# Optimization experiments

Hardware: AMD Instinct MI355X
Metric: run time of the kernel (lower is better)

Reference implementation:

```python
import jax, jax.numpy as jnp
import numpy as np

D_MODEL = 1024
NUM_HEADS = 16
HEAD_DIM = D_MODEL // NUM_HEADS  # 64
# NOTE: the original module passes scale=attention_head_size, so scores are
# MULTIPLIED by head_dim (64), not divided by sqrt(head_dim). Faithful quirk.
SCALE = float(HEAD_DIM)


def setup_inputs() -> dict:
    key = jax.random.key(0)
    ks = jax.random.split(key, 6)
    bs, s, d = 2, 2048, D_MODEL
    q = jax.random.normal(ks[0], (bs, s, d), dtype=jnp.float32)
    k = jax.random.normal(ks[1], (bs, s, d), dtype=jnp.float32)
    v = jax.random.normal(ks[2], (bs, s, d), dtype=jnp.float32)
    # nn.Linear weights, shape (out, in); no bias (qkv_bias=False)
    init = 1.0 / np.sqrt(d)
    Wq = jax.random.uniform(ks[3], (d, d), jnp.float32, -init, init)
    Wk = jax.random.uniform(ks[4], (d, d), jnp.float32, -init, init)
    Wv = jax.random.uniform(ks[5], (d, d), jnp.float32, -init, init)
    return {"q": q, "k": k, "v": v, "Wq": Wq, "Wk": Wk, "Wv": Wv}


def _split_heads(x):
    bs, s, _ = x.shape
    return x.reshape(bs, s, NUM_HEADS, HEAD_DIM).transpose(0, 2, 1, 3)  # bhsd


def reference(q, k, v, Wq, Wk, Wv):
    bs, s, d = q.shape
    qh = _split_heads(q @ Wq.T)  # [b,h,s,hd]
    kh = _split_heads(k @ Wk.T)
    vh = _split_heads(v @ Wv.T)
    sims = jnp.einsum('bhqd,bhkd->bhqk', qh, kh) * SCALE
    attn = jax.nn.softmax(sims, axis=-1)
    out = jnp.einsum('bhqk,bhkd->bhqd', attn, vh)  # [b,h,s,hd]
    out = out.transpose(0, 2, 1, 3).reshape(bs, s, d)
    return out
```

## Files before the change

kernel.cpp:

```cpp
#include <hip/hip_runtime.h>


typedef _Float16 half4 __attribute__((ext_vector_type(4)));
typedef _Float16 half8 __attribute__((ext_vector_type(8)));
typedef float floatx4 __attribute__((ext_vector_type(4)));

#define MFMA_F16(a, b, c) __builtin_amdgcn_mfma_f32_16x16x32_f16((a), (b), (c), 0, 0, 0)

constexpr int SEQ = 2048;
constexpr int DM = 1024;
constexpr int NH = 16;
constexpr int HD = 64;
constexpr float QSCALE = 92.33248261689366f;

__device__ __forceinline__ void gl2lds16(const _Float16* g, _Float16* l) {
  __builtin_amdgcn_global_load_lds(
      (const __attribute__((address_space(1))) void*)g,
      (__attribute__((address_space(3))) void*)l, 16, 0, 0);
}

__device__ inline void split4(const float4 f, half4& h, half4& l) {
  h[0] = (_Float16)f.x; l[0] = (_Float16)(f.x - (float)h[0]);
  h[1] = (_Float16)f.y; l[1] = (_Float16)(f.y - (float)h[1]);
  h[2] = (_Float16)f.z; l[2] = (_Float16)(f.z - (float)h[2]);
  h[3] = (_Float16)f.w; l[3] = (_Float16)(f.w - (float)h[3]);
}

__global__ __launch_bounds__(256) void convert_all(
    const float* __restrict__ q, const float* __restrict__ k,
    const float* __restrict__ v, const float* __restrict__ Wq,
    const float* __restrict__ Wk, const float* __restrict__ Wv,
    _Float16* __restrict__ xq_h, _Float16* __restrict__ xq_l,
    _Float16* __restrict__ xk_h, _Float16* __restrict__ xk_l,
    _Float16* __restrict__ xv_h,
    _Float16* __restrict__ Wqh, _Float16* __restrict__ Wql,
    _Float16* __restrict__ Wkh, _Float16* __restrict__ Wkl,
    _Float16* __restrict__ Wvh)
{
  const int bid = blockIdx.x;
  const float* src; _Float16* dh; _Float16* dl; int do_lo, i0;
  if (bid < 4096)       { src = q;  dh = xq_h; dl = xq_l; do_lo = 1; i0 = bid; }
  else if (bid < 8192)  { src = k;  dh = xk_h; dl = xk_l; do_lo = 1; i0 = bid - 4096; }
  else if (bid < 12288) { src = v;  dh = xv_h; dl = xv_h; do_lo = 0; i0 = bid - 8192; }
  else if (bid < 13312) { src = Wq; dh = Wqh;  dl = Wql;  do_lo = 1; i0 = bid - 12288; }
  else if (bid < 14336) { src = Wk; dh = Wkh;  dl = Wkl;  do_lo = 1; i0 = bid - 13312; }
  else                  { src = Wv; dh = Wvh;  dl = Wvh;  do_lo = 0; i0 = bid - 14336; }
  const int idx = i0 * 256 + threadIdx.x;
  float4 f = ((const float4*)src)[idx];
  half4 h, l; split4(f, h, l);
  *(half4*)(dh + (size_t)idx * 4) = h;
  if (do_lo) *(half4*)(dl + (size_t)idx * 4) = l;
}

__global__ __launch_bounds__(256, 1) void proj3_kernel(
    const _Float16* __restrict__ xq_h, const _Float16* __restrict__ xq_l,
    const _Float16* __restrict__ xk_h, const _Float16* __restrict__ xk_l,
    const _Float16* __restrict__ xv_h,
    const _Float16* __restrict__ Wqh, const _Float16* __restrict__ Wql,
    const _Float16* __restrict__ Wkh, const _Float16* __restrict__ Wkl,
    const _Float16* __restrict__ Wvh,
    _Float16* __restrict__ qh_hi, _Float16* __restrict__ qh_lo,
    _Float16* __restrict__ kh_hi, _Float16* __restrict__ kh_lo,
    _Float16* __restrict__ vhT)
{
  __shared__ __align__(16) _Float16 Ahs[128][64];
  __shared__ __align__(16) _Float16 Als[128][64];
  __shared__ __align__(16) _Float16 Bhs[128][64];
  __shared__ __align__(16) _Float16 Bls[128][64];

  const int z = blockIdx.z;
  const _Float16 *Ahg, *Alg, *Bhg, *Blg;
  _Float16 *yh, *yl;
  float scale; int three;
  if (z == 0)      { Ahg = xq_h; Alg = xq_l; Bhg = Wqh; Blg = Wql;
                     yh = qh_hi; yl = qh_lo; scale = QSCALE; three = 1; }
  else if (z == 1) { Ahg = xk_h; Alg = xk_l; Bhg = Wkh; Blg = Wkl;
                     yh = kh_hi; yl = kh_lo; scale = 1.0f; three = 1; }
  else             { Ahg = xv_h; Alg = xv_h; Bhg = Wvh; Blg = Wvh;
                     yh = vhT;   yl = vhT;   scale = 1.0f; three = 0; }

  const int tid = threadIdx.x;
  const int bm = blockIdx.x;
  const int bn = blockIdx.y;
  const int lane = tid & 63, l15 = lane & 15, quad = lane >> 4;
  const int w = tid >> 6, wm = w >> 1, wn = w & 1;

  const int r8 = lane >> 3;
  const int cp8 = (((lane & 7) ^ r8)) * 8;
  int grow[4]; _Float16* la[4]; _Float16* lal[4]; _Float16* lb[4]; _Float16* lbl[4];
  #pragma unroll
  for (int i = 0; i < 4; i++) {
    const int g = w * 4 + i;
    grow[i] = g * 8 + r8;
    la[i]  = &Ahs[0][0] + g * 512;
    lal[i] = &Als[0][0] + g * 512;
    lb[i]  = &Bhs[0][0] + g * 512;
    lbl[i] = &Bls[0][0] + g * 512;
  }

  floatx4 acc[4][4];
  #pragma unroll
  for (int mt = 0; mt < 4; mt++)
    #pragma unroll
    for (int nt = 0; nt < 4; nt++)
      acc[mt][nt] = (floatx4){0.f, 0.f, 0.f, 0.f};

  for (int kk = 0; kk < DM; kk += 64) {
    __syncthreads();
    #pragma unroll
    for (int i = 0; i < 4; i++) {
      const size_t ga = (size_t)(bm * 128 + grow[i]) * DM + kk + cp8;
      const size_t gb = (size_t)(bn * 128 + grow[i]) * DM + kk + cp8;
      gl2lds16(Ahg + ga, la[i]);
      gl2lds16(Bhg + gb, lb[i]);
      if (three) {
        gl2lds16(Alg + ga, lal[i]);
        gl2lds16(Blg + gb, lbl[i]);
      }
    }
    __syncthreads();

    #pragma unroll
    for (int kc = 0; kc < 2; kc++) {
      const int swz = ((kc * 4 + quad) ^ (l15 & 7)) * 8;
      half8 ah[4], bh_[4], al[4], bl[4];
      #pragma unroll
      for (int t = 0; t < 4; t++) {
        ah[t]  = *(const half8*)&Ahs[wm * 64 + t * 16 + l15][swz];
        bh_[t] = *(const half8*)&Bhs[wn * 64 + t * 16 + l15][swz];
        if (three) {
          al[t] = *(const half8*)&Als[wm * 64 + t * 16 + l15][swz];
          bl[t] = *(const half8*)&Bls[wn * 64 + t * 16 + l15][swz];
        }
      }
      if (three) {
        #pragma unroll
        for (int mt = 0; mt < 4; mt++)
          #pragma unroll
          for (int nt = 0; nt < 4; nt++) {
            floatx4 t0 = MFMA_F16(ah[mt], bh_[nt], acc[mt][nt]);
            t0 = MFMA_F16(ah[mt], bl[nt], t0);
            acc[mt][nt] = MFMA_F16(al[mt], bh_[nt], t0);
          }
      } else {
        #pragma unroll
        for (int mt = 0; mt < 4; mt++)
          #pragma unroll
          for (int nt = 0; nt < 4; nt++)
            acc[mt][nt] = MFMA_F16(ah[mt], bh_[nt], acc[mt][nt]);
      }
    }
  }

  if (three) {
    #pragma unroll
    for (int mt = 0; mt < 4; mt++)
      #pragma unroll
      for (int nt = 0; nt < 4; nt++)
        #pragma unroll
        for (int r = 0; r < 4; r++) {
          int gm = bm * 128 + wm * 64 + mt * 16 + quad * 4 + r;
          int gn = bn * 128 + wn * 64 + nt * 16 + l15;
          int b = gm >> 11, s = gm & 2047;
          int h = gn >> 6, d = gn & 63;
          size_t idx = ((size_t)(b * NH + h) * SEQ + s) * HD + d;
          float val = acc[mt][nt][r] * scale;
          _Float16 hi = (_Float16)val;
          yh[idx] = hi;
          yl[idx] = (_Float16)(val - (float)hi);
        }
  } else {
    const int b = bm >> 4;
    const int h = bn * 2 + wn;
    const int bh = b * NH + h;
    const int sbase = (bm & 15) * 128 + wm * 64;
    _Float16* vt = vhT + (size_t)bh * HD * SEQ;
    #pragma unroll
    for (int mt = 0; mt < 4; mt++) {
      const int pos = sbase + (mt >> 1) * 32 + quad * 8 + (mt & 1) * 4;
      #pragma unroll
      for (int nt = 0; nt < 4; nt++) {
        const int d = nt * 16 + l15;
        half4 hv;
        hv[0] = (_Float16)acc[mt][nt][0];
        hv[1] = (_Float16)acc[mt][nt][1];
        hv[2] = (_Float16)acc[mt][nt][2];
        hv[3] = (_Float16)acc[mt][nt][3];
        *(half4*)(vt + (size_t)d * SEQ + pos) = hv;
      }
    }
  }
}

__global__ __launch_bounds__(256, 4) void flash_kernel(
    const _Float16* __restrict__ qh_hi, const _Float16* __restrict__ qh_lo,
    const _Float16* __restrict__ kh_hi, const _Float16* __restrict__ kh_lo,
    const _Float16* __restrict__ vhT, float* __restrict__ Op, float2* __restrict__ ml)
{
  __shared__ __align__(16) _Float16 Kh[2][64][64];
  __shared__ __align__(16) _Float16 Kl[2][64][64];
  __shared__ __align__(16) _Float16 Vt[64][64];

  const int id = blockIdx.x;
  const int seq_ = id >> 3;
  const int bh = (id & 7) + 8 * (seq_ & 3);
  const int rem = seq_ >> 2;
  const int qb = rem & 15;
  const int kh = rem >> 4;
  const int tid = threadIdx.x;
  const int wq = tid >> 6;
  const int lane = tid & 63, l15 = lane & 15, quad = lane >> 4;

  const size_t bh_off = (size_t)bh * SEQ * HD;
  const _Float16* __restrict__ kh_p = kh_hi + bh_off;
  const _Float16* __restrict__ kl_p = kh_lo + bh_off;
  const _Float16* __restrict__ vt_p = vhT + (size_t)bh * HD * SEQ;
  const int qrow0 = qb * 128 + wq * 32;

  half8 bqh[2][2], bql[2][2];
  #pragma unroll
  for (int g = 0; g < 2; g++) {
    const _Float16* qp_h = qh_hi + bh_off + (size_t)(qrow0 + g * 16 + l15) * HD;
    const _Float16* qp_l = qh_lo + bh_off + (size_t)(qrow0 + g * 16 + l15) * HD;
    #pragma unroll
    for (int kc = 0; kc < 2; kc++) {
      bqh[g][kc] = *(const half8*)(qp_h + kc * 32 + quad * 8);
      bql[g][kc] = *(const half8*)(qp_l + kc * 32 + quad * 8);
    }
  }

  const int r8 = lane >> 3;
  const int cp8 = ((lane & 7) ^ r8) * 8;

  float m_[2] = {-3.0e38f, -3.0e38f};
  float l_[2] = {0.f, 0.f};
  floatx4 Oacc[2][4];
  #pragma unroll
  for (int g = 0; g < 2; g++)
    #pragma unroll
    for (int nd = 0; nd < 4; nd++) Oacc[g][nd] = (floatx4){0.f, 0.f, 0.f, 0.f};

  const int kt0 = kh * 16;
  {
    const int kbase = kt0 * 64;
    #pragma unroll
    for (int i = 0; i < 2; i++) {
      const int g = wq * 2 + i;
      const int r = g * 8 + r8;
      gl2lds16(kh_p + (size_t)(kbase + r) * HD + cp8, &Kh[0][0][0] + g * 512);
      gl2lds16(kl_p + (size_t)(kbase + r) * HD + cp8, &Kl[0][0][0] + g * 512);
    }
  }

  for (int kt = kt0; kt < kt0 + 16; kt++) {
    const int cur = kt & 1;
    const int kbase = kt * 64;
    __syncthreads();

    #pragma unroll
    for (int i = 0; i < 2; i++) {
      const int g = wq * 2 + i;
      const int r = g * 8 + r8;
      gl2lds16(vt_p + (size_t)r * SEQ + kbase + cp8, &Vt[0][0] + g * 512);
    }
    if (kt + 1 < kt0 + 16) {
      const int kb2 = (kt + 1) * 64, nxt = cur ^ 1;
      #pragma unroll
      for (int i = 0; i < 2; i++) {
        const int g = wq * 2 + i;
        const int r = g * 8 + r8;
        gl2lds16(kh_p + (size_t)(kb2 + r) * HD + cp8, &Kh[nxt][0][0] + g * 512);
        gl2lds16(kl_p + (size_t)(kb2 + r) * HD + cp8, &Kl[nxt][0][0] + g * 512);
      }
    }

    floatx4 sacc[2][4];
    const int r7 = l15 & 7;
    #pragma unroll
    for (int nt = 0; nt < 4; nt++) {
      half8 akh0 = *(const half8*)&Kh[cur][nt * 16 + l15][((0 * 4 + quad) ^ r7) * 8];
      half8 akh1 = *(const half8*)&Kh[cur][nt * 16 + l15][((1 * 4 + quad) ^ r7) * 8];
      half8 akl0 = *(const half8*)&Kl[cur][nt * 16 + l15][((0 * 4 + quad) ^ r7) * 8];
      half8 akl1 = *(const half8*)&Kl[cur][nt * 16 + l15][((1 * 4 + quad) ^ r7) * 8];
      #pragma unroll
      for (int g = 0; g < 2; g++) {
        floatx4 s4 = (floatx4){0.f, 0.f, 0.f, 0.f};
        s4 = MFMA_F16(akh0, bqh[g][0], s4);
        s4 = MFMA_F16(akh1, bqh[g][1], s4);
        s4 = MFMA_F16(akh0, bql[g][0], s4);
        s4 = MFMA_F16(akh1, bql[g][1], s4);
        s4 = MFMA_F16(akl0, bqh[g][0], s4);
        s4 = MFMA_F16(akl1, bqh[g][1], s4);
        sacc[g][nt] = s4;
      }
    }

    float alpha2[2];
    half8 bp8g[2][2];
    #pragma unroll
    for (int g = 0; g < 2; g++) {
      float rmax = sacc[g][0][0];
      #pragma unroll
      for (int nt = 0; nt < 4; nt++)
        #pragma unroll
        for (int r = 0; r < 4; r++) rmax = fmaxf(rmax, sacc[g][nt][r]);
      rmax = fmaxf(rmax, __shfl_xor(rmax, 16, 64));
      rmax = fmaxf(rmax, __shfl_xor(rmax, 32, 64));
      const float mnew = fmaxf(m_[g], rmax);
      alpha2[g] = exp2f(m_[g] - mnew);
      m_[g] = mnew;

      float rsum = 0.f;
      #pragma unroll
      for (int nt = 0; nt < 4; nt++)
        #pragma unroll
        for (int r = 0; r < 4; r++) {
          float p = exp2f(sacc[g][nt][r] - mnew);
          sacc[g][nt][r] = p;
          rsum += p;
        }
      rsum += __shfl_xor(rsum, 16, 64);
      rsum += __shfl_xor(rsum, 32, 64);
      l_[g] = l_[g] * alpha2[g] + rsum;

      #pragma unroll
      for (int kc = 0; kc < 2; kc++)
        #pragma unroll
        for (int j = 0; j < 8; j++)
          bp8g[g][kc][j] = (_Float16)sacc[g][2 * kc + (j >> 2)][j & 3];
    }

    __syncthreads();

    half8 av[4][2];
    #pragma unroll
    for (int nd = 0; nd < 4; nd++) {
      av[nd][0] = *(const half8*)&Vt[nd * 16 + l15][((0 * 4 + quad) ^ r7) * 8];
      av[nd][1] = *(const half8*)&Vt[nd * 16 + l15][((1 * 4 + quad) ^ r7) * 8];
    }

    #pragma unroll
    for (int g = 0; g < 2; g++) {
      #pragma unroll
      for (int nd = 0; nd < 4; nd++) {
        Oacc[g][nd][0] *= alpha2[g]; Oacc[g][nd][1] *= alpha2[g];
        Oacc[g][nd][2] *= alpha2[g]; Oacc[g][nd][3] *= alpha2[g];
        Oacc[g][nd] = MFMA_F16(av[nd][0], bp8g[g][0], Oacc[g][nd]);
        Oacc[g][nd] = MFMA_F16(av[nd][1], bp8g[g][1], Oacc[g][nd]);
      }
    }
  }

  const size_t fqbase = (size_t)bh * SEQ + qrow0;
  #pragma unroll
  for (int g = 0; g < 2; g++) {
    const size_t fq = fqbase + g * 16 + l15;
    float* ob = Op + ((size_t)kh * 65536 + fq) * HD;
    #pragma unroll
    for (int nd = 0; nd < 4; nd++) {
      float4 vv;
      vv.x = Oacc[g][nd][0]; vv.y = Oacc[g][nd][1];
      vv.z = Oacc[g][nd][2]; vv.w = Oacc[g][nd][3];
      *(float4*)(ob + nd * 16 + quad * 4) = vv;
    }
    if (quad == 0) ml[kh * 65536 + fq] = make_float2(m_[g], l_[g]);
  }
}

__global__ __launch_bounds__(256) void merge_kernel(const float* __restrict__ Op,
                                                    const float2* __restrict__ ml,
                                                    float* __restrict__ out)
{
  const int tid = threadIdx.x;
  const int fq = blockIdx.x * 64 + (tid >> 2);
  const int dp = (tid & 3) * 16;
  float2 m0 = ml[fq], m1 = ml[65536 + fq];
  float M = fmaxf(m0.x, m1.x);
  float w0 = exp2f(m0.x - M), w1 = exp2f(m1.x - M);
  float rinv = 1.0f / (m0.y * w0 + m1.y * w1);
  int bh = fq >> 11, s = fq & 2047, b = bh >> 4, h = bh & 15;
  float* ob = out + ((size_t)(b * SEQ + s)) * DM + h * HD + dp;
  const float* p0 = Op + (size_t)fq * HD + dp;
  const float* p1 = p0 + (size_t)65536 * HD;
  #pragma unroll
  for (int j = 0; j < 4; j++) {
    float4 a = *(const float4*)(p0 + 4 * j);
    float4 c = *(const float4*)(p1 + 4 * j);
    float4 r;
    r.x = (a.x * w0 + c.x * w1) * rinv;
    r.y = (a.y * w0 + c.y * w1) * rinv;
    r.z = (a.z * w0 + c.z * w1) * rinv;
    r.w = (a.w * w0 + c.w * w1) * rinv;
    *(float4*)(ob + 4 * j) = r;
  }
}

extern "C" void kernel_launch(void* const* d_in, const int* in_sizes, int n_in,
                              void* d_out, int out_size, void* d_ws, size_t ws_size,
                              hipStream_t stream) {
  const float* q  = (const float*)d_in[0];
  const float* k  = (const float*)d_in[1];
  const float* v  = (const float*)d_in[2];
  const float* Wq = (const float*)d_in[3];
  const float* Wk = (const float*)d_in[4];
  const float* Wv = (const float*)d_in[5];
  float* out = (float*)d_out;

  char* W = (char*)d_ws;
  const size_t MiB = 1ull << 20;
  _Float16* qh_hi = (_Float16*)(W + 0 * MiB);
  _Float16* qh_lo = (_Float16*)(W + 8 * MiB);
  _Float16* kh_hi = (_Float16*)(W + 16 * MiB);
  _Float16* kh_lo = (_Float16*)(W + 24 * MiB);
  _Float16* vhT   = (_Float16*)(W + 32 * MiB);
  _Float16* xq_h  = (_Float16*)(W + 48 * MiB);
  _Float16* xq_l  = (_Float16*)(W + 56 * MiB);
  _Float16* xk_h  = (_Float16*)(W + 64 * MiB);
  _Float16* xk_l  = (_Float16*)(W + 72 * MiB);
  _Float16* xv_h  = (_Float16*)(W + 80 * MiB);
  _Float16* Wqh   = (_Float16*)(W + 88 * MiB);
  _Float16* Wql   = (_Float16*)(W + 90 * MiB);
  _Float16* Wkh   = (_Float16*)(W + 92 * MiB);
  _Float16* Wkl   = (_Float16*)(W + 94 * MiB);
  _Float16* Wvh   = (_Float16*)(W + 96 * MiB);
  float*    Op    = (float*)  (W + 40 * MiB);
  float2*   mlp   = (float2*) (W + 98 * MiB);

  convert_all<<<15360, 256, 0, stream>>>(q, k, v, Wq, Wk, Wv,
                                         xq_h, xq_l, xk_h, xk_l, xv_h,
                                         Wqh, Wql, Wkh, Wkl, Wvh);
  proj3_kernel<<<dim3(32, 8, 3), 256, 0, stream>>>(
      xq_h, xq_l, xk_h, xk_l, xv_h, Wqh, Wql, Wkh, Wkl, Wvh,
      qh_hi, qh_lo, kh_hi, kh_lo, vhT);
  flash_kernel<<<1024, 256, 0, stream>>>(qh_hi, qh_lo, kh_hi, kh_lo, vhT, Op, mlp);
  merge_kernel<<<1024, 256, 0, stream>>>(Op, mlp, out);
}
```

Baseline: 286.6 us.

## Stage projection epilogue through LDS, compute softmax row sums via MFMA

The Q/K projection epilogue now stages the hi/lo fp16 results in shared memory and writes them to global as coalesced 16-byte vectors instead of scattered 2-byte stores. In the attention kernel the row-sum reduction (VALU adds plus two shuffles) is replaced by an MFMA against a ones vector over the fp16 probabilities, which moves work to the matrix unit. The row max now uses a three-input max pattern. The risks are that the sum is taken over fp16-rounded probabilities, and that the epilogue adds several barriers.

```diff
diff --git a/kernel.cpp b/kernel.cpp
--- a/kernel.cpp
+++ b/kernel.cpp
@@ -12,6 +12,10 @@
 constexpr int NH = 16;
 constexpr int HD = 64;
 constexpr float QSCALE = 92.33248261689366f;
+
+__device__ __forceinline__ float fmax3(float a, float b, float c) {
+  return fmaxf(fmaxf(a, b), c);
+}
 
 __device__ __forceinline__ void gl2lds16(const _Float16* g, _Float16* l) {
   __builtin_amdgcn_global_load_lds(
@@ -63,10 +67,11 @@
     _Float16* __restrict__ kh_hi, _Float16* __restrict__ kh_lo,
     _Float16* __restrict__ vhT)
 {
-  __shared__ __align__(16) _Float16 Ahs[128][64];
-  __shared__ __align__(16) _Float16 Als[128][64];
-  __shared__ __align__(16) _Float16 Bhs[128][64];
-  __shared__ __align__(16) _Float16 Bls[128][64];
+  __shared__ __align__(16) _Float16 smem[4 * 128 * 64];
+  _Float16* Ahs = smem;
+  _Float16* Als = smem + 8192;
+  _Float16* Bhs = smem + 16384;
+  _Float16* Bls = smem + 24576;
 
   const int z = blockIdx.z;
   const _Float16 *Ahg, *Alg, *Bhg, *Blg;
@@ -92,10 +97,10 @@
   for (int i = 0; i < 4; i++) {
     const int g = w * 4 + i;
     grow[i] = g * 8 + r8;
-    la[i]  = &Ahs[0][0] + g * 512;
-    lal[i] = &Als[0][0] + g * 512;
-    lb[i]  = &Bhs[0][0] + g * 512;
-    lbl[i] = &Bls[0][0] + g * 512;
+    la[i]  = Ahs + g * 512;
+    lal[i] = Als + g * 512;
+    lb[i]  = Bhs + g * 512;
+    lbl[i] = Bls + g * 512;
   }
 
   floatx4 acc[4][4];
@@ -126,11 +131,11 @@
       half8 ah[4], bh_[4], al[4], bl[4];
       #pragma unroll
       for (int t = 0; t < 4; t++) {
-        ah[t]  = *(const half8*)&Ahs[wm * 64 + t * 16 + l15][swz];
-        bh_[t] = *(const half8*)&Bhs[wn * 64 + t * 16 + l15][swz];
+        ah[t]  = *(const half8*)&Ahs[(wm * 64 + t * 16 + l15) * 64 + swz];
+        bh_[t] = *(const half8*)&Bhs[(wn * 64 + t * 16 + l15) * 64 + swz];
         if (three) {
-          al[t] = *(const half8*)&Als[wm * 64 + t * 16 + l15][swz];
-          bl[t] = *(const half8*)&Bls[wn * 64 + t * 16 + l15][swz];
+          al[t] = *(const half8*)&Als[(wm * 64 + t * 16 + l15) * 64 + swz];
+          bl[t] = *(const half8*)&Bls[(wn * 64 + t * 16 + l15) * 64 + swz];
         }
       }
       if (three) {
@@ -153,22 +158,44 @@
   }
 
   if (three) {
-    #pragma unroll
-    for (int mt = 0; mt < 4; mt++)
-      #pragma unroll
-      for (int nt = 0; nt < 4; nt++)
-        #pragma unroll
-        for (int r = 0; r < 4; r++) {
-          int gm = bm * 128 + wm * 64 + mt * 16 + quad * 4 + r;
-          int gn = bn * 128 + wn * 64 + nt * 16 + l15;
-          int b = gm >> 11, s = gm & 2047;
-          int h = gn >> 6, d = gn & 63;
-          size_t idx = ((size_t)(b * NH + h) * SEQ + s) * HD + d;
-          float val = acc[mt][nt][r] * scale;
-          _Float16 hi = (_Float16)val;
-          yh[idx] = hi;
-          yl[idx] = (_Float16)(val - (float)hi);
+    _Float16 (*E)[136] = (_Float16(*)[136])smem;
+    const int rrow = tid >> 2;
+    const int chunk = tid & 3;
+    const int eh = chunk >> 1;
+    const int d0 = (chunk & 1) * 32;
+    __syncthreads();
+    #pragma unroll
+    for (int half = 0; half < 2; half++) {
+      #pragma unroll
+      for (int part = 0; part < 2; part++) {
+        if (wm == half) {
+          #pragma unroll
+          for (int mt = 0; mt < 4; mt++)
+            #pragma unroll
+            for (int nt = 0; nt < 4; nt++)
+              #pragma unroll
+              for (int r = 0; r < 4; r++) {
+                const int rl = mt * 16 + quad * 4 + r;
+                const int c = wn * 64 + nt * 16 + l15;
+                float val = acc[mt][nt][r] * scale;
+                _Float16 hi = (_Float16)val;
+                E[rl][c] = part ? (_Float16)(val - (float)hi) : hi;
+              }
         }
+        __syncthreads();
+        const int gm = bm * 128 + half * 64 + rrow;
+        const int b = gm >> 11, s = gm & 2047;
+        const int h = bn * 2 + eh;
+        _Float16* dst = (part ? yl : yh) +
+                        ((size_t)(b * NH + h) * SEQ + s) * HD + d0;
+        const int c0 = chunk * 32;
+        *(half8*)(dst)      = *(const half8*)&E[rrow][c0];
+        *(half8*)(dst + 8)  = *(const half8*)&E[rrow][c0 + 8];
+        *(half8*)(dst + 16) = *(const half8*)&E[rrow][c0 + 16];
+        *(half8*)(dst + 24) = *(const half8*)&E[rrow][c0 + 24];
+        __syncthreads();
+      }
+    }
   } else {
     const int b = bm >> 4;
     const int h = bn * 2 + wn;
@@ -229,6 +256,10 @@
     }
   }
 
+  half8 onesA;
+  #pragma unroll
+  for (int j = 0; j < 8; j++) onesA[j] = (l15 == 0) ? (_Float16)1.0f : (_Float16)0.0f;
+
   const int r8 = lane >> 3;
   const int cp8 = ((lane & 7) ^ r8) * 8;
 
@@ -299,29 +330,25 @@
     half8 bp8g[2][2];
     #pragma unroll
     for (int g = 0; g < 2; g++) {
-      float rmax = sacc[g][0][0];
-      #pragma unroll
-      for (int nt = 0; nt < 4; nt++)
-        #pragma unroll
-        for (int r = 0; r < 4; r++) rmax = fmaxf(rmax, sacc[g][nt][r]);
+      #define SG(i) sacc[g][(i) >> 2][(i) & 3]
+      float t0 = fmax3(SG(0), SG(1), SG(2));
+      float t1 = fmax3(SG(3), SG(4), SG(5));
+      float t2 = fmax3(SG(6), SG(7), SG(8));
+      float t3 = fmax3(SG(9), SG(10), SG(11));
+      float t4 = fmax3(SG(12), SG(13), SG(14));
+      float rmax = fmaxf(fmax3(t0, t1, t2), fmax3(t3, t4, SG(15)));
+      #undef SG
       rmax = fmaxf(rmax, __shfl_xor(rmax, 16, 64));
       rmax = fmaxf(rmax, __shfl_xor(rmax, 32, 64));
       const float mnew = fmaxf(m_[g], rmax);
       alpha2[g] = exp2f(m_[g] - mnew);
       m_[g] = mnew;
 
-      float rsum = 0.f;
       #pragma unroll
       for (int nt = 0; nt < 4; nt++)
         #pragma unroll
-        for (int r = 0; r < 4; r++) {
-          float p = exp2f(sacc[g][nt][r] - mnew);
-          sacc[g][nt][r] = p;
-          rsum += p;
-        }
-      rsum += __shfl_xor(rsum, 16, 64);
-      rsum += __shfl_xor(rsum, 32, 64);
-      l_[g] = l_[g] * alpha2[g] + rsum;
+        for (int r = 0; r < 4; r++)
+          sacc[g][nt][r] = exp2f(sacc[g][nt][r] - mnew);
 
       #pragma unroll
       for (int kc = 0; kc < 2; kc++)
@@ -348,6 +375,10 @@
         Oacc[g][nd] = MFMA_F16(av[nd][0], bp8g[g][0], Oacc[g][nd]);
         Oacc[g][nd] = MFMA_F16(av[nd][1], bp8g[g][1], Oacc[g][nd]);
       }
+      floatx4 accL = (floatx4){0.f, 0.f, 0.f, 0.f};
+      accL = MFMA_F16(onesA, bp8g[g][0], accL);
+      accL = MFMA_F16(onesA, bp8g[g][1], accL);
+      l_[g] = l_[g] * alpha2[g] + accL[0];
     }
   }
 
```

Measured after the change: 297.5 us. +3.8%, slower.

## Split attention keys four ways, store fp16 partials, single-buffer LDS tiles

Applied to the files above, without the earlier changes.

Each query block's key range is now split four ways instead of two, doubling the flash-kernel grid to 2048 blocks and halving the key tiles per block. The aim is more parallelism and occupancy, helped by raising launch bounds to 6 and dropping the double-buffered K/Kl LDS arrays. Partial outputs are stored as fp16 instead of fp32, so the intermediate written and then read back by the merge kernel stays the same size despite twice as many splits. The merge kernel is templated on the split count. The costs are lost prefetch overlap, since tiles now load, sync, then compute, and extra rounding in the partial outputs.

```diff
diff --git a/kernel.cpp b/kernel.cpp
--- a/kernel.cpp
+++ b/kernel.cpp
@@ -192,19 +192,21 @@
   }
 }
 
-__global__ __launch_bounds__(256, 4) void flash_kernel(
+template<int KSPLIT>
+__global__ __launch_bounds__(256, 6) void flash_kernel(
     const _Float16* __restrict__ qh_hi, const _Float16* __restrict__ qh_lo,
     const _Float16* __restrict__ kh_hi, const _Float16* __restrict__ kh_lo,
-    const _Float16* __restrict__ vhT, float* __restrict__ Op, float2* __restrict__ ml)
+    const _Float16* __restrict__ vhT, _Float16* __restrict__ Op,
+    float2* __restrict__ ml)
 {
-  __shared__ __align__(16) _Float16 Kh[2][64][64];
-  __shared__ __align__(16) _Float16 Kl[2][64][64];
+  __shared__ __align__(16) _Float16 Kh[64][64];
+  __shared__ __align__(16) _Float16 Kl[64][64];
   __shared__ __align__(16) _Float16 Vt[64][64];
 
+  constexpr int NKT = 32 / KSPLIT;
   const int id = blockIdx.x;
-  const int seq_ = id >> 3;
-  const int bh = (id & 7) + 8 * (seq_ & 3);
-  const int rem = seq_ >> 2;
+  const int bh = (id & 7) + 8 * ((id >> 3) & 3);
+  const int rem = id >> 5;
   const int qb = rem & 15;
   const int kh = rem >> 4;
   const int tid = threadIdx.x;
@@ -240,48 +242,28 @@
     #pragma unroll
     for (int nd = 0; nd < 4; nd++) Oacc[g][nd] = (floatx4){0.f, 0.f, 0.f, 0.f};
 
-  const int kt0 = kh * 16;
-  {
-    const int kbase = kt0 * 64;
+  const int kt0 = kh * NKT;
+  for (int kt = kt0; kt < kt0 + NKT; kt++) {
+    const int kbase = kt * 64;
+    __syncthreads();
     #pragma unroll
     for (int i = 0; i < 2; i++) {
       const int g = wq * 2 + i;
       const int r = g * 8 + r8;
-      gl2lds16(kh_p + (size_t)(kbase + r) * HD + cp8, &Kh[0][0][0] + g * 512);
-      gl2lds16(kl_p + (size_t)(kbase + r) * HD + cp8, &Kl[0][0][0] + g * 512);
-    }
-  }
-
-  for (int kt = kt0; kt < kt0 + 16; kt++) {
-    const int cur = kt & 1;
-    const int kbase = kt * 64;
+      gl2lds16(kh_p + (size_t)(kbase + r) * HD + cp8, &Kh[0][0] + g * 512);
+      gl2lds16(kl_p + (size_t)(kbase + r) * HD + cp8, &Kl[0][0] + g * 512);
+      gl2lds16(vt_p + (size_t)r * SEQ + kbase + cp8, &Vt[0][0] + g * 512);
+    }
     __syncthreads();
-
-    #pragma unroll
-    for (int i = 0; i < 2; i++) {
-      const int g = wq * 2 + i;
-      const int r = g * 8 + r8;
-      gl2lds16(vt_p + (size_t)r * SEQ + kbase + cp8, &Vt[0][0] + g * 512);
-    }
-    if (kt + 1 < kt0 + 16) {
-      const int kb2 = (kt + 1) * 64, nxt = cur ^ 1;
-      #pragma unroll
-      for (int i = 0; i < 2; i++) {
-        const int g = wq * 2 + i;
-        const int r = g * 8 + r8;
-        gl2lds16(kh_p + (size_t)(kb2 + r) * HD + cp8, &Kh[nxt][0][0] + g * 512);
-        gl2lds16(kl_p + (size_t)(kb2 + r) * HD + cp8, &Kl[nxt][0][0] + g * 512);
-      }
-    }
 
     floatx4 sacc[2][4];
     const int r7 = l15 & 7;
     #pragma unroll
     for (int nt = 0; nt < 4; nt++) {
-      half8 akh0 = *(const half8*)&Kh[cur][nt * 16 + l15][((0 * 4 + quad) ^ r7) * 8];
-      half8 akh1 = *(const half8*)&Kh[cur][nt * 16 + l15][((1 * 4 + quad) ^ r7) * 8];
-      half8 akl0 = *(const half8*)&Kl[cur][nt * 16 + l15][((0 * 4 + quad) ^ r7) * 8];
-      half8 akl1 = *(const half8*)&Kl[cur][nt * 16 + l15][((1 * 4 + quad) ^ r7) * 8];
+      half8 akh0 = *(const half8*)&Kh[nt * 16 + l15][((0 * 4 + quad) ^ r7) * 8];
+      half8 akh1 = *(const half8*)&Kh[nt * 16 + l15][((1 * 4 + quad) ^ r7) * 8];
+      half8 akl0 = *(const half8*)&Kl[nt * 16 + l15][((0 * 4 + quad) ^ r7) * 8];
+      half8 akl1 = *(const half8*)&Kl[nt * 16 + l15][((1 * 4 + quad) ^ r7) * 8];
       #pragma unroll
       for (int g = 0; g < 2; g++) {
         floatx4 s4 = (floatx4){0.f, 0.f, 0.f, 0.f};
@@ -295,8 +277,13 @@
       }
     }
 
-    float alpha2[2];
-    half8 bp8g[2][2];
+    half8 av[4][2];
+    #pragma unroll
+    for (int nd = 0; nd < 4; nd++) {
+      av[nd][0] = *(const half8*)&Vt[nd * 16 + l15][((0 * 4 + quad) ^ r7) * 8];
+      av[nd][1] = *(const half8*)&Vt[nd * 16 + l15][((1 * 4 + quad) ^ r7) * 8];
+    }
+
     #pragma unroll
     for (int g = 0; g < 2; g++) {
       float rmax = sacc[g][0][0];
@@ -307,7 +294,7 @@
       rmax = fmaxf(rmax, __shfl_xor(rmax, 16, 64));
       rmax = fmaxf(rmax, __shfl_xor(rmax, 32, 64));
       const float mnew = fmaxf(m_[g], rmax);
-      alpha2[g] = exp2f(m_[g] - mnew);
+      const float alpha = exp2f(m_[g] - mnew);
       m_[g] = mnew;
 
       float rsum = 0.f;
@@ -321,32 +308,21 @@
         }
       rsum += __shfl_xor(rsum, 16, 64);
       rsum += __shfl_xor(rsum, 32, 64);
-      l_[g] = l_[g] * alpha2[g] + rsum;
-
+      l_[g] = l_[g] * alpha + rsum;
+
+      half8 bp8[2];
       #pragma unroll
       for (int kc = 0; kc < 2; kc++)
         #pragma unroll
         for (int j = 0; j < 8; j++)
-          bp8g[g][kc][j] = (_Float16)sacc[g][2 * kc + (j >> 2)][j & 3];
-    }
-
-    __syncthreads();
-
-    half8 av[4][2];
-    #pragma unroll
-    for (int nd = 0; nd < 4; nd++) {
-      av[nd][0] = *(const half8*)&Vt[nd * 16 + l15][((0 * 4 + quad) ^ r7) * 8];
-      av[nd][1] = *(const half8*)&Vt[nd * 16 + l15][((1 * 4 + quad) ^ r7) * 8];
-    }
-
-    #pragma unroll
-    for (int g = 0; g < 2; g++) {
+          bp8[kc][j] = (_Float16)sacc[g][2 * kc + (j >> 2)][j & 3];
+
       #pragma unroll
       for (int nd = 0; nd < 4; nd++) {
-        Oacc[g][nd][0] *= alpha2[g]; Oacc[g][nd][1] *= alpha2[g];
-        Oacc[g][nd][2] *= alpha2[g]; Oacc[g][nd][3] *= alpha2[g];
-        Oacc[g][nd] = MFMA_F16(av[nd][0], bp8g[g][0], Oacc[g][nd]);
-        Oacc[g][nd] = MFMA_F16(av[nd][1], bp8g[g][1], Oacc[g][nd]);
+        Oacc[g][nd][0] *= alpha; Oacc[g][nd][1] *= alpha;
+        Oacc[g][nd][2] *= alpha; Oacc[g][nd][3] *= alpha;
+        Oacc[g][nd] = MFMA_F16(av[nd][0], bp8[0], Oacc[g][nd]);
+        Oacc[g][nd] = MFMA_F16(av[nd][1], bp8[1], Oacc[g][nd]);
       }
     }
   }
@@ -355,42 +331,53 @@
   #pragma unroll
   for (int g = 0; g < 2; g++) {
     const size_t fq = fqbase + g * 16 + l15;
-    float* ob = Op + ((size_t)kh * 65536 + fq) * HD;
+    _Float16* ob = Op + ((size_t)kh * 65536 + fq) * HD;
     #pragma unroll
     for (int nd = 0; nd < 4; nd++) {
-      float4 vv;
-      vv.x = Oacc[g][nd][0]; vv.y = Oacc[g][nd][1];
-      vv.z = Oacc[g][nd][2]; vv.w = Oacc[g][nd][3];
-      *(float4*)(ob + nd * 16 + quad * 4) = vv;
+      half4 hv;
+      hv[0] = (_Float16)Oacc[g][nd][0]; hv[1] = (_Float16)Oacc[g][nd][1];
+      hv[2] = (_Float16)Oacc[g][nd][2]; hv[3] = (_Float16)Oacc[g][nd][3];
+      *(half4*)(ob + nd * 16 + quad * 4) = hv;
     }
     if (quad == 0) ml[kh * 65536 + fq] = make_float2(m_[g], l_[g]);
   }
 }
 
-__global__ __launch_bounds__(256) void merge_kernel(const float* __restrict__ Op,
+template<int KSPLIT>
+__global__ __launch_bounds__(256) void merge_kernel(const _Float16* __restrict__ Op,
                                                     const float2* __restrict__ ml,
                                                     float* __restrict__ out)
 {
   const int tid = threadIdx.x;
   const int fq = blockIdx.x * 64 + (tid >> 2);
   const int dp = (tid & 3) * 16;
-  float2 m0 = ml[fq], m1 = ml[65536 + fq];
-  float M = fmaxf(m0.x, m1.x);
-  float w0 = exp2f(m0.x - M), w1 = exp2f(m1.x - M);
-  float rinv = 1.0f / (m0.y * w0 + m1.y * w1);
-  int bh = fq >> 11, s = fq & 2047, b = bh >> 4, h = bh & 15;
-  float* ob = out + ((size_t)(b * SEQ + s)) * DM + h * HD + dp;
-  const float* p0 = Op + (size_t)fq * HD + dp;
-  const float* p1 = p0 + (size_t)65536 * HD;
+  float2 mls[KSPLIT];
+  float M = -3.0e38f;
+  #pragma unroll
+  for (int s = 0; s < KSPLIT; s++) {
+    mls[s] = ml[s * 65536 + fq];
+    M = fmaxf(M, mls[s].x);
+  }
+  float wsum = 0.f, w[KSPLIT];
+  #pragma unroll
+  for (int s = 0; s < KSPLIT; s++) {
+    w[s] = exp2f(mls[s].x - M);
+    wsum += mls[s].y * w[s];
+  }
+  const float rinv = 1.0f / wsum;
+  int bh = fq >> 11, sq = fq & 2047, b = bh >> 4, h = bh & 15;
+  float* ob = out + ((size_t)(b * SEQ + sq)) * DM + h * HD + dp;
+  const _Float16* p0 = Op + (size_t)fq * HD + dp;
   #pragma unroll
   for (int j = 0; j < 4; j++) {
-    float4 a = *(const float4*)(p0 + 4 * j);
-    float4 c = *(const float4*)(p1 + 4 * j);
-    float4 r;
-    r.x = (a.x * w0 + c.x * w1) * rinv;
-    r.y = (a.y * w0 + c.y * w1) * rinv;
-    r.z = (a.z * w0 + c.z * w1) * rinv;
-    r.w = (a.w * w0 + c.w * w1) * rinv;
+    float4 r = make_float4(0.f, 0.f, 0.f, 0.f);
+    #pragma unroll
+    for (int s = 0; s < KSPLIT; s++) {
+      half4 a = *(const half4*)(p0 + (size_t)s * 65536 * HD + 4 * j);
+      r.x += (float)a[0] * w[s]; r.y += (float)a[1] * w[s];
+      r.z += (float)a[2] * w[s]; r.w += (float)a[3] * w[s];
+    }
+    r.x *= rinv; r.y *= rinv; r.z *= rinv; r.w *= rinv;
     *(float4*)(ob + 4 * j) = r;
   }
 }
@@ -423,7 +410,7 @@
   _Float16* Wkh   = (_Float16*)(W + 92 * MiB);
   _Float16* Wkl   = (_Float16*)(W + 94 * MiB);
   _Float16* Wvh   = (_Float16*)(W + 96 * MiB);
-  float*    Op    = (float*)  (W + 40 * MiB);
+  _Float16* Op    = (_Float16*)(W + 40 * MiB);
   float2*   mlp   = (float2*) (W + 98 * MiB);
 
   convert_all<<<15360, 256, 0, stream>>>(q, k, v, Wq, Wk, Wv,
@@ -432,6 +419,6 @@
   proj3_kernel<<<dim3(32, 8, 3), 256, 0, stream>>>(
       xq_h, xq_l, xk_h, xk_l, xv_h, Wqh, Wql, Wkh, Wkl, Wvh,
       qh_hi, qh_lo, kh_hi, kh_lo, vhT);
-  flash_kernel<<<1024, 256, 0, stream>>>(qh_hi, qh_lo, kh_hi, kh_lo, vhT, Op, mlp);
-  merge_kernel<<<1024, 256, 0, stream>>>(Op, mlp, out);
-}
+  flash_kernel<4><<<2048, 256, 0, stream>>>(qh_hi, qh_lo, kh_hi, kh_lo, vhT, Op, mlp);
+  merge_kernel<4><<<1024, 256, 0, stream>>>(Op, mlp, out);
+}
```

Result: slower. 671.3 us (+134.2%).
